# Optimization experiments

Hardware: AMD Instinct MI355X
Metric: run time of the kernel (lower is better)

Reference implementation:

```python
import jax, jax.numpy as jnp
import numpy as np

T, B, C, K, E = 1024, 32, 1024, 1024, 16  # seq, batch, d_model(=in=out), key_dim, n_experts
LOSS_SCALE = 0.01


def setup_inputs() -> dict:
    key0 = jax.random.key(0)
    k0, k1, k2, k3 = jax.random.split(key0, 4)
    x = jax.random.normal(k0, (T, B, C), dtype=jnp.float32)
    key = jax.random.normal(k1, (1, B, K), dtype=jnp.float32)
    bnd = float(np.sqrt(6.0 / (K + E)))  # xavier_uniform for assign Linear
    assign_w = jax.random.uniform(k2, (K, E), jnp.float32, -bnd, bnd)
    assign_b = jnp.zeros((E,), jnp.float32)
    a = float(np.sqrt(6.0) / (C + C))  # dynamic_init_method=1
    pw_w1 = jax.random.uniform(k3, (E, C * C), jnp.float32, -a, a)
    return {"x": x, "key": key, "assign_w": assign_w, "assign_b": assign_b, "pw_w1": pw_w1}


def reference(x, key, assign_w, assign_b, pw_w1):
    Tn, Bn, Cn = x.shape
    Tr = key.shape[0]  # key is provided -> Tr = 1 (one routing decision per batch element)
    En = assign_b.shape[0]
    # routing: softmax over experts (gumbel_tau=0 -> plain softmax branch)
    logits = key.reshape(Tr * Bn, -1) @ assign_w + assign_b  # (Tr*B, E)
    resp = jax.nn.softmax(logits, axis=-1)
    importance = resp.sum(axis=0)  # (E,)
    loss = LOSS_SCALE * jnp.std(importance, ddof=1) / jnp.mean(importance)  # torch.std is unbiased
    # mix expert weights: (Tr*B, E) @ (E, O*I) -> per-token/sentence weight matrix
    w = (resp @ pw_w1).reshape(Tr, Bn, Cn, Cn)  # (Tr, B, O, I)
    # batched matvec, broadcasting Tr=1 over T (sum over size-1 axis r == broadcast)
    y = jnp.einsum('rboi,tbi->tbo', w, x)
    return x + y, loss
```

## Files before the change

### kernel.cpp

```cpp
#include <hip/hip_runtime.h>
#include <stdint.h>


#define TBC   (1024*32*1024)

typedef __attribute__((ext_vector_type(8))) __bf16 bf16x8;
typedef __attribute__((ext_vector_type(4))) float  floatx4;

#define XSWZ(r) ((((r) & 3) ^ (((r) >> 2) & 3)))

__device__ __forceinline__ unsigned short f2bf(float f) {
  unsigned u = __float_as_uint(f);
  unsigned r = u + 0x7fffu + ((u >> 16) & 1u);
  return (unsigned short)(r >> 16);
}
__device__ __forceinline__ float bf2f(unsigned short u) {
  return __uint_as_float(((unsigned)u) << 16);
}

__device__ __forceinline__ void async16(const void* g, void* l) {
  __builtin_amdgcn_global_load_lds(
      (const __attribute__((address_space(1))) void*)(unsigned long long)(uintptr_t)g,
      (__attribute__((address_space(3))) void*)(unsigned int)(uintptr_t)l,
      16, 0, 0);
}

__global__ __launch_bounds__(256) void routing_kernel(
    const float* __restrict__ key, const float* __restrict__ aw,
    const float* __restrict__ ab, float* __restrict__ resp) {
  __shared__ float part[16][17];
  __shared__ float logit[16];
  const int b = blockIdx.x;
  const int tid = threadIdx.x;
  const int e = tid & 15, ks = tid >> 4;
  const float* kb = key + b * 1024 + ks * 64;
  float acc = 0.f;
  #pragma unroll 8
  for (int k = 0; k < 64; ++k)
    acc = fmaf(kb[k], aw[(ks * 64 + k) * 16 + e], acc);
  part[e][ks] = acc;
  __syncthreads();
  if (tid < 16) {
    float s = ab[tid];
    #pragma unroll
    for (int j = 0; j < 16; ++j) s += part[tid][j];
    logit[tid] = s;
  }
  __syncthreads();
  if (tid < 16) {
    float m = logit[0];
    #pragma unroll
    for (int j = 1; j < 16; ++j) m = fmaxf(m, logit[j]);
    float s = 0.f;
    #pragma unroll
    for (int j = 0; j < 16; ++j) s += expf(logit[j] - m);
    resp[b * 16 + tid] = expf(logit[tid] - m) / s;
  }
}

__global__ void loss_kernel(const float* __restrict__ resp, float* __restrict__ loss_out) {
  __shared__ float imp[16];
  const int tid = threadIdx.x;
  if (tid < 16) {
    float s = 0.f;
    for (int bb = 0; bb < 32; ++bb) s += resp[bb * 16 + tid];
    imp[tid] = s;
  }
  __syncthreads();
  if (tid == 0) {
    float mu = 0.f;
    for (int j = 0; j < 16; ++j) mu += imp[j];
    mu *= (1.f / 16.f);
    float var = 0.f;
    for (int j = 0; j < 16; ++j) { float d = imp[j] - mu; var += d * d; }
    var *= (1.f / 15.f);
    loss_out[0] = 0.01f * sqrtf(var) / mu;
  }
}

__global__ __launch_bounds__(256) void prep_kernel(
    const float4* __restrict__ x, ushort4* __restrict__ xb,
    const float4* __restrict__ pw, const float* __restrict__ resp,
    ushort4* __restrict__ W) {
  const int tid = threadIdx.x;
  if (blockIdx.x < 2048) {
    const int base = blockIdx.x * 256 + tid;
    #pragma unroll
    for (int j = 0; j < 16; ++j) {
      const int i = base + j * 524288;
      float4 v = x[i];
      ushort4 o;
      o.x = f2bf(v.x); o.y = f2bf(v.y); o.z = f2bf(v.z); o.w = f2bf(v.w);
      xb[i] = o;
    }
  } else {
    __shared__ float rs[512];
    rs[tid] = resp[tid];
    rs[tid + 256] = resp[tid + 256];
    __syncthreads();
    const int p = (blockIdx.x - 2048) * 256 + tid;
    float4 v[16];
    #pragma unroll
    for (int e = 0; e < 16; ++e) v[e] = pw[e * 262144 + p];
    #pragma unroll
    for (int b = 0; b < 32; ++b) {
      float ax = 0.f, ay = 0.f, az = 0.f, aww = 0.f;
      #pragma unroll
      for (int e = 0; e < 16; ++e) {
        const float r = rs[b * 16 + e];
        ax = fmaf(r, v[e].x, ax); ay = fmaf(r, v[e].y, ay);
        az = fmaf(r, v[e].z, az); aww = fmaf(r, v[e].w, aww);
      }
      ushort4 o;
      o.x = f2bf(ax); o.y = f2bf(ay); o.z = f2bf(az); o.w = f2bf(aww);
      W[(size_t)b * 262144 + p] = o;
    }
  }
}

__global__ __launch_bounds__(512, 2) void gemm_kernel(
    const unsigned short* __restrict__ xb,
    const unsigned short* __restrict__ Wb,
    float* __restrict__ out) {
  __shared__ unsigned short lds[4][2][8192];
  const int tid  = threadIdx.x;
  const int lane = tid & 63;
  const int wave = tid >> 6;
  const int wm = wave >> 2;
  const int wn = wave & 3;

  const int gid   = blockIdx.x;
  const int xcd   = gid & 7;
  const int local = gid >> 3;
  const int b     = xcd * 4 + (local >> 4);
  const int sub   = local & 15;
  const int t0    = (sub >> 2) * 256;
  const int o0    = (sub & 3) * 256;

  const unsigned short* gA[2];
  const unsigned short* gB[2];
  #pragma unroll
  for (int j = 0; j < 2; ++j) {
    const int s  = j * 512 + tid;
    const int r  = s >> 2;
    const int cg = (s & 3) ^ XSWZ(r);
    gA[j] = xb + (size_t)(t0 + r) * 32768 + (size_t)b * 1024 + cg * 8;
    gB[j] = Wb + (size_t)b * 1048576 + (size_t)(o0 + r) * 1024 + cg * 8;
  }

  floatx4 acc[8][4];
  #pragma unroll
  for (int a = 0; a < 8; ++a)
    #pragma unroll
    for (int ni = 0; ni < 4; ++ni)
      acc[a][ni] = floatx4{0.f, 0.f, 0.f, 0.f};

  auto stage = [&](int bufi) {
    #pragma unroll
    for (int j = 0; j < 2; ++j) {
      const int dst = (j * 512 + wave * 64) * 8;
      async16(gA[j], &lds[bufi][0][dst]);
      async16(gB[j], &lds[bufi][1][dst]);
      gA[j] += 32; gB[j] += 32;
    }
  };

  auto compute = [&](int bufi) {
    const unsigned short* lA = &lds[bufi][0][0];
    const unsigned short* lB = &lds[bufi][1][0];
    bf16x8 bfr[4];
    #pragma unroll
    for (int ni = 0; ni < 4; ++ni) {
      const int r = wn * 64 + ni * 16 + (lane & 15);
      const int slot = (lane >> 4) ^ XSWZ(r);
      bfr[ni] = *(const bf16x8*)(lB + r * 32 + slot * 8);
    }
    #pragma unroll
    for (int half = 0; half < 2; ++half) {
      bf16x8 afr[4];
      #pragma unroll
      for (int mi = 0; mi < 4; ++mi) {
        const int r = wm * 128 + half * 64 + mi * 16 + (lane & 15);
        const int slot = (lane >> 4) ^ XSWZ(r);
        afr[mi] = *(const bf16x8*)(lA + r * 32 + slot * 8);
      }
      __builtin_amdgcn_s_setprio(1);
      #pragma unroll
      for (int mi = 0; mi < 4; ++mi)
        #pragma unroll
        for (int ni = 0; ni < 4; ++ni)
          acc[half * 4 + mi][ni] = __builtin_amdgcn_mfma_f32_16x16x32_bf16(
              afr[mi], bfr[ni], acc[half * 4 + mi][ni], 0, 0, 0);
      __builtin_amdgcn_s_setprio(0);
      if (half == 0) __builtin_amdgcn_s_barrier();
    }
  };

  stage(0); stage(1); stage(2);

  for (int t = 0; t < 32; ++t) {
    if (t <= 28) {
      stage((t + 3) & 3);
      asm volatile("s_waitcnt vmcnt(12)" ::: "memory");
    } else if (t == 29) {
      asm volatile("s_waitcnt vmcnt(8)" ::: "memory");
    } else if (t == 30) {
      asm volatile("s_waitcnt vmcnt(4)" ::: "memory");
    } else {
      asm volatile("s_waitcnt vmcnt(0)" ::: "memory");
    }
    __builtin_amdgcn_s_barrier();
    asm volatile("" ::: "memory");
    compute(t & 3);
    asm volatile("s_waitcnt lgkmcnt(0)" ::: "memory");
    __builtin_amdgcn_s_barrier();
  }

  #pragma unroll
  for (int a = 0; a < 8; ++a) {
    const int tb = t0 + wm * 128 + (a >> 2) * 64 + (a & 3) * 16 + (lane >> 4) * 4;
    #pragma unroll
    for (int ni = 0; ni < 4; ++ni) {
      const int o = o0 + wn * 64 + ni * 16 + (lane & 15);
      #pragma unroll
      for (int v = 0; v < 4; ++v) {
        const size_t idx = (size_t)(tb + v) * 32768 + (size_t)b * 1024 + o;
        out[idx] = acc[a][ni][v] + bf2f(xb[idx]);
      }
    }
  }
}

extern "C" void kernel_launch(void* const* d_in, const int* in_sizes, int n_in,
                              void* d_out, int out_size, void* d_ws, size_t ws_size,
                              hipStream_t stream) {
  const float* x   = (const float*)d_in[0];
  const float* key = (const float*)d_in[1];
  const float* aw  = (const float*)d_in[2];
  const float* ab  = (const float*)d_in[3];
  const float* pw  = (const float*)d_in[4];
  float* out = (float*)d_out;

  char* ws = (char*)d_ws;
  unsigned short* Wb = (unsigned short*)ws;
  unsigned short* xb = (unsigned short*)(ws + 67108864);
  float* resp        = (float*)(ws + 134217728);

  routing_kernel<<<32, 256, 0, stream>>>(key, aw, ab, resp);
  loss_kernel<<<1, 64, 0, stream>>>(resp, out + TBC);
  prep_kernel<<<3072, 256, 0, stream>>>((const float4*)x, (ushort4*)xb,
                                        (const float4*)pw, resp, (ushort4*)Wb);
  gemm_kernel<<<512, 512, 0, stream>>>(xb, Wb, out);
}
```

Measured before the change: 410.0 us.

## Regroup prep kernels: fuse x conversion with routing, loss with weight mixing

Moves the x fp32-to-bf16 conversion into the routing kernel as extra blocks, and folds the loss computation into the expert-weight mixing kernel. The launch sequence shrinks from four kernels to three, and the large x conversion now runs alongside routing instead of behind it. Per-thread work in the conversion path changes from 16 to 8 float4s. Adds a launch_bounds occupancy hint on the mixing kernel.

After: 402.9 us. Within noise of the previous version (-1.7%).

```diff
diff --git a/kernel.cpp b/kernel.cpp
--- a/kernel.cpp
+++ b/kernel.cpp
@@ -25,13 +25,26 @@
       16, 0, 0);
 }
 
-__global__ __launch_bounds__(256) void routing_kernel(
+__global__ __launch_bounds__(256) void route_conv_kernel(
     const float* __restrict__ key, const float* __restrict__ aw,
-    const float* __restrict__ ab, float* __restrict__ resp) {
+    const float* __restrict__ ab, float* __restrict__ resp,
+    const float4* __restrict__ x, ushort4* __restrict__ xb) {
+  const int tid = threadIdx.x;
+  if (blockIdx.x >= 32) {
+    const int i0 = (blockIdx.x - 32) * 256 + tid;
+    #pragma unroll
+    for (int j = 0; j < 8; ++j) {
+      const int i = i0 + j * 1048576;
+      float4 v = x[i];
+      ushort4 o;
+      o.x = f2bf(v.x); o.y = f2bf(v.y); o.z = f2bf(v.z); o.w = f2bf(v.w);
+      xb[i] = o;
+    }
+    return;
+  }
   __shared__ float part[16][17];
   __shared__ float logit[16];
   const int b = blockIdx.x;
-  const int tid = threadIdx.x;
   const int e = tid & 15, ks = tid >> 4;
   const float* kb = key + b * 1024 + ks * 64;
   float acc = 0.f;
@@ -58,63 +71,46 @@
   }
 }
 
-__global__ void loss_kernel(const float* __restrict__ resp, float* __restrict__ loss_out) {
-  __shared__ float imp[16];
+__global__ __launch_bounds__(256, 4) void mix_loss_kernel(
+    const float4* __restrict__ pw, const float* __restrict__ resp,
+    ushort4* __restrict__ W, float* __restrict__ loss_out) {
+  __shared__ float rs[512];
   const int tid = threadIdx.x;
-  if (tid < 16) {
-    float s = 0.f;
-    for (int bb = 0; bb < 32; ++bb) s += resp[bb * 16 + tid];
-    imp[tid] = s;
-  }
+  rs[tid] = resp[tid];
+  rs[tid + 256] = resp[tid + 256];
   __syncthreads();
-  if (tid == 0) {
+  if (blockIdx.x == 0 && tid == 0) {
+    float imp[16];
     float mu = 0.f;
-    for (int j = 0; j < 16; ++j) mu += imp[j];
+    #pragma unroll
+    for (int e = 0; e < 16; ++e) {
+      float s = 0.f;
+      for (int bb = 0; bb < 32; ++bb) s += rs[bb * 16 + e];
+      imp[e] = s; mu += s;
+    }
     mu *= (1.f / 16.f);
     float var = 0.f;
-    for (int j = 0; j < 16; ++j) { float d = imp[j] - mu; var += d * d; }
+    #pragma unroll
+    for (int e = 0; e < 16; ++e) { float d = imp[e] - mu; var += d * d; }
     var *= (1.f / 15.f);
     loss_out[0] = 0.01f * sqrtf(var) / mu;
   }
-}
-
-__global__ __launch_bounds__(256) void prep_kernel(
-    const float4* __restrict__ x, ushort4* __restrict__ xb,
-    const float4* __restrict__ pw, const float* __restrict__ resp,
-    ushort4* __restrict__ W) {
-  const int tid = threadIdx.x;
-  if (blockIdx.x < 2048) {
-    const int base = blockIdx.x * 256 + tid;
-    #pragma unroll
-    for (int j = 0; j < 16; ++j) {
-      const int i = base + j * 524288;
-      float4 v = x[i];
-      ushort4 o;
-      o.x = f2bf(v.x); o.y = f2bf(v.y); o.z = f2bf(v.z); o.w = f2bf(v.w);
-      xb[i] = o;
-    }
-  } else {
-    __shared__ float rs[512];
-    rs[tid] = resp[tid];
-    rs[tid + 256] = resp[tid + 256];
-    __syncthreads();
-    const int p = (blockIdx.x - 2048) * 256 + tid;
-    float4 v[16];
-    #pragma unroll
-    for (int e = 0; e < 16; ++e) v[e] = pw[e * 262144 + p];
-    #pragma unroll
-    for (int b = 0; b < 32; ++b) {
-      float ax = 0.f, ay = 0.f, az = 0.f, aww = 0.f;
-      #pragma unroll
-      for (int e = 0; e < 16; ++e) {
-        const float r = rs[b * 16 + e];
-        ax = fmaf(r, v[e].x, ax); ay = fmaf(r, v[e].y, ay);
-        az = fmaf(r, v[e].z, az); aww = fmaf(r, v[e].w, aww);
-      }
-      ushort4 o;
-      o.x = f2bf(ax); o.y = f2bf(ay); o.z = f2bf(az); o.w = f2bf(aww);
-      W[(size_t)b * 262144 + p] = o;
-    }
+  const int p = blockIdx.x * 256 + tid;
+  float4 v[16];
+  #pragma unroll
+  for (int e = 0; e < 16; ++e) v[e] = pw[e * 262144 + p];
+  #pragma unroll
+  for (int b = 0; b < 32; ++b) {
+    float ax = 0.f, ay = 0.f, az = 0.f, aww = 0.f;
+    #pragma unroll
+    for (int e = 0; e < 16; ++e) {
+      const float r = rs[b * 16 + e];
+      ax = fmaf(r, v[e].x, ax); ay = fmaf(r, v[e].y, ay);
+      az = fmaf(r, v[e].z, az); aww = fmaf(r, v[e].w, aww);
+    }
+    ushort4 o;
+    o.x = f2bf(ax); o.y = f2bf(ay); o.z = f2bf(az); o.w = f2bf(aww);
+    W[(size_t)b * 262144 + p] = o;
   }
 }
 
@@ -246,9 +242,9 @@
   unsigned short* xb = (unsigned short*)(ws + 67108864);
   float* resp        = (float*)(ws + 134217728);
 
-  routing_kernel<<<32, 256, 0, stream>>>(key, aw, ab, resp);
-  loss_kernel<<<1, 64, 0, stream>>>(resp, out + TBC);
-  prep_kernel<<<3072, 256, 0, stream>>>((const float4*)x, (ushort4*)xb,
-                                        (const float4*)pw, resp, (ushort4*)Wb);
+  route_conv_kernel<<<4128, 256, 0, stream>>>(key, aw, ab, resp,
+                                              (const float4*)x, (ushort4*)xb);
+  mix_loss_kernel<<<1024, 256, 0, stream>>>((const float4*)pw, resp,
+                                            (ushort4*)Wb, out + TBC);
   gemm_kernel<<<512, 512, 0, stream>>>(xb, Wb, out);
 }
```
